# Kernel tuning notes

Hardware: AMD Instinct MI355X
Metric: run time of the kernel (lower is better)

Reference implementation:

```python
import jax, jax.numpy as jnp
import numpy as np

DIM = 768
N_HEADS = 12
HEAD_DIM = DIM // N_HEADS
HIDDEN = 4 * DIM
EPS = 1e-5


def _layernorm(x, gamma, beta):
    mu = jnp.mean(x, axis=-1, keepdims=True)
    var = jnp.mean(jnp.square(x - mu), axis=-1, keepdims=True)
    return (x - mu) * jax.lax.rsqrt(var + EPS) * gamma + beta


def setup_inputs() -> dict:
    key = jax.random.key(0)
    ks = jax.random.split(key, 8)
    B, N = 16, 1024
    s = 0.02
    return {
        "x": jax.random.normal(ks[0], (B, N, DIM), jnp.float32),
        "Wqkv": jax.random.normal(ks[1], (DIM, 3 * DIM), jnp.float32) * s,
        "bqkv": jnp.zeros((3 * DIM,), jnp.float32),
        "Wproj": jax.random.normal(ks[2], (DIM, DIM), jnp.float32) * s,
        "bproj": jnp.zeros((DIM,), jnp.float32),
        "g1": jnp.ones((DIM,), jnp.float32),
        "b1": jnp.zeros((DIM,), jnp.float32),
        "g2": jnp.ones((DIM,), jnp.float32),
        "b2": jnp.zeros((DIM,), jnp.float32),
        "W1": jax.random.normal(ks[3], (DIM, HIDDEN), jnp.float32) * s,
        "bf1": jnp.zeros((HIDDEN,), jnp.float32),
        "W2": jax.random.normal(ks[4], (HIDDEN, DIM), jnp.float32) * s,
        "bf2": jnp.zeros((DIM,), jnp.float32),
    }


def reference(x, Wqkv, bqkv, Wproj, bproj, g1, b1, g2, b2, W1, bf1, W2, bf2):
    B, N, _ = x.shape
    # --- attention branch (pre-LN) ---
    h = _layernorm(x, g1, b1)
    qkv = (h @ Wqkv + bqkv).reshape(B, N, 3, N_HEADS, HEAD_DIM)
    qkv = jnp.transpose(qkv, (2, 0, 3, 1, 4))  # [3, B, H, N, D]
    q, k, v = qkv[0], qkv[1], qkv[2]
    # NOTE: source scales by dim**-0.5, not head_dim**-0.5 (faithful)
    scores = jnp.einsum("bhnd,bhmd->bhnm", q, k) * (DIM ** -0.5)
    attn = jax.nn.softmax(scores, axis=-1)
    out = jnp.einsum("bhnm,bhmd->bhnd", attn, v)
    out = jnp.transpose(out, (0, 2, 1, 3)).reshape(B, N, DIM)
    x = x + (out @ Wproj + bproj)
    # --- MLP branch ---
    h2 = _layernorm(x, g2, b2)
    ff = jax.nn.relu(h2 @ W1 + bf1) @ W2 + bf2
    return x + ff
```

## Files before the change

kernel.cpp:

```cpp
#include <hip/hip_runtime.h>
#include <cstdint>
#include <cstddef>

typedef unsigned short u16;
typedef __bf16 bf16x8 __attribute__((ext_vector_type(8)));
typedef unsigned short u16x8 __attribute__((ext_vector_type(8)));
typedef float f32x4 __attribute__((ext_vector_type(4)));

#define DIMN 768
#define BNROWS 16384
#define NH 12
#define HD 64
#define HID 3072
#define QKVN 2304

__device__ __forceinline__ u16 f2bf(float f) {
  unsigned u = __builtin_bit_cast(unsigned, f);
  u += 0x7fffu + ((u >> 16) & 1u);
  return (u16)(u >> 16);
}

__device__ __forceinline__ bf16x8 ld8(const u16* p) {
  u16x8 v = *reinterpret_cast<const u16x8*>(p);
  return __builtin_bit_cast(bf16x8, v);
}

__device__ __forceinline__ void gload16(const void* g, void* l) {
  __builtin_amdgcn_global_load_lds(
      (const __attribute__((address_space(1))) unsigned int*)g,
      (__attribute__((address_space(3))) unsigned int*)l, 16, 0, 0);
}

#define MFMA(a, b, c) __builtin_amdgcn_mfma_f32_16x16x32_bf16(a, b, c, 0, 0, 0)

__global__ __launch_bounds__(256) void twb_k(const float* __restrict__ W,
                                             u16* __restrict__ Wt, int K, int N) {
  __shared__ float tile[32][33];
  const int n0 = blockIdx.x * 32, k0 = blockIdx.y * 32;
  const int tx = threadIdx.x & 31, ty = threadIdx.x >> 5;
#pragma unroll
  for (int i = 0; i < 4; i++)
    tile[ty + i * 8][tx] = W[(size_t)(k0 + ty + i * 8) * N + n0 + tx];
  __syncthreads();
#pragma unroll
  for (int i = 0; i < 4; i++)
    Wt[(size_t)(n0 + ty + i * 8) * K + k0 + tx] = f2bf(tile[tx][ty + i * 8]);
}

__global__ __launch_bounds__(256) void ln_k(const float* __restrict__ x,
                                            const float* __restrict__ g,
                                            const float* __restrict__ bta,
                                            u16* __restrict__ outp) {
  const int row = blockIdx.x * 4 + (threadIdx.x >> 6);
  const int lane = threadIdx.x & 63;
  const float4* xr = (const float4*)(x + (size_t)row * DIMN);
  float4 v[3];
  float s = 0.f, ss = 0.f;
#pragma unroll
  for (int c = 0; c < 3; c++) {
    v[c] = xr[c * 64 + lane];
    s += v[c].x + v[c].y + v[c].z + v[c].w;
    ss += v[c].x * v[c].x + v[c].y * v[c].y + v[c].z * v[c].z + v[c].w * v[c].w;
  }
#pragma unroll
  for (int off = 1; off < 64; off <<= 1) {
    s += __shfl_xor(s, off);
    ss += __shfl_xor(ss, off);
  }
  const float mu = s * (1.f / DIMN);
  const float var = ss * (1.f / DIMN) - mu * mu;
  const float rs = rsqrtf(var + 1e-5f);
  u16* orow = outp + (size_t)row * DIMN;
#pragma unroll
  for (int c = 0; c < 3; c++) {
    float4 gv = ((const float4*)g)[c * 64 + lane];
    float4 bv = ((const float4*)bta)[c * 64 + lane];
    ushort4 o;
    o.x = f2bf((v[c].x - mu) * rs * gv.x + bv.x);
    o.y = f2bf((v[c].y - mu) * rs * gv.y + bv.y);
    o.z = f2bf((v[c].z - mu) * rs * gv.z + bv.z);
    o.w = f2bf((v[c].w - mu) * rs * gv.w + bv.w);
    ((ushort4*)orow)[c * 64 + lane] = o;
  }
}

template <int OUT_BF16, int RELU, int RESID>
__global__ __launch_bounds__(512, 2) void gemm256_k(const u16* __restrict__ A,
                                                    const u16* __restrict__ Bt,
                                                    const float* __restrict__ bias,
                                                    const float* __restrict__ resid,
                                                    void* __restrict__ Cout, int N, int K) {
  __shared__ u16 lds[65536];
  const int tid = threadIdx.x;
  const int m0 = blockIdx.x * 256;
  const int n0 = blockIdx.y * 256;
  const int lane = tid & 63, w = tid >> 6;
  const int wr = w >> 2, wc = w & 3;
  const int lhi = lane >> 4, llo = lane & 15;
  const int rdoff = (lhi ^ ((llo >> 1) & 3)) * 16;
  const int NT = K >> 5;

  const int srow = tid >> 2;
  const int sc8 = ((tid & 3) ^ ((srow >> 1) & 3)) * 8;
  const u16* aS0 = A + (size_t)(m0 + srow) * K + sc8;
  const u16* aS1 = A + (size_t)(m0 + 128 + srow) * K + sc8;
  const u16* bS0 = Bt + (size_t)(n0 + srow) * K + sc8;
  const u16* bS1 = Bt + (size_t)(n0 + 128 + srow) * K + sc8;

  auto slotBase = [&](int t) -> const char* { return (const char*)lds + ((size_t)(t & 3) << 15); };
  auto stageA = [&](int t) {
    char* sb = (char*)lds + ((size_t)(t & 3) << 15);
    gload16(aS0 + t * 32, sb + tid * 16);
    gload16(aS1 + t * 32, sb + 8192 + tid * 16);
  };
  auto stageB = [&](int t) {
    char* sb = (char*)lds + ((size_t)(t & 3) << 15) + 16384;
    gload16(bS0 + t * 32, sb + tid * 16);
    gload16(bS1 + t * 32, sb + 8192 + tid * 16);
  };

  f32x4 acc[8][4] = {};
  bf16x8 a03[2][4], bfr[2][4], a47[4];

  stageB(0); stageA(0);
  stageB(1); stageA(1);
  stageB(2); stageA(2);
  asm volatile("s_waitcnt vmcnt(8)" ::: "memory");
  __builtin_amdgcn_s_barrier();
  {
    const char* sb = slotBase(0);
#pragma unroll
    for (int ni = 0; ni < 4; ni++)
      bfr[0][ni] = ld8((const u16*)(sb + 16384 + (wc * 64 + ni * 16 + llo) * 64 + rdoff));
#pragma unroll
    for (int mi = 0; mi < 4; mi++)
      a03[0][mi] = ld8((const u16*)(sb + (wr * 128 + mi * 16 + llo) * 64 + rdoff));
  }

#define G256_P1(T, CUR)                                                                  \
  {                                                                                      \
    const char* sbp = slotBase(T);                                                       \
    _Pragma("unroll") for (int mi = 0; mi < 4; mi++)                                     \
        a47[mi] = ld8((const u16*)(sbp + (wr * 128 + (4 + mi) * 16 + llo) * 64 + rdoff));\
    if ((T) + 3 < NT) stageB((T) + 3);                                                   \
    if ((T) + 3 < NT) {                                                                  \
      asm volatile("s_waitcnt vmcnt(6)" ::: "memory");                                   \
    } else if ((T) + 2 < NT) {                                                           \
      asm volatile("s_waitcnt vmcnt(4)" ::: "memory");                                   \
    } else if ((T) + 1 < NT) {                                                           \
      asm volatile("s_waitcnt vmcnt(0)" ::: "memory");                                   \
    }                                                                                    \
    __builtin_amdgcn_s_barrier();                                                        \
    asm volatile("s_waitcnt lgkmcnt(4)" ::: "memory");                                   \
    __builtin_amdgcn_sched_barrier(0);                                                   \
    __builtin_amdgcn_s_setprio(1);                                                       \
    _Pragma("unroll") for (int mi = 0; mi < 4; mi++)                                     \
        _Pragma("unroll") for (int ni = 0; ni < 4; ni++)                                 \
            acc[mi][ni] = MFMA(a03[CUR][mi], bfr[CUR][ni], acc[mi][ni]);                 \
    __builtin_amdgcn_s_setprio(0);                                                       \
    __builtin_amdgcn_sched_barrier(0);                                                   \
  }

#define G256_P2(T, CUR, NXT)                                                             \
  {                                                                                      \
    if ((T) + 1 < NT) {                                                                  \
      const char* sbn = slotBase((T) + 1);                                               \
      _Pragma("unroll") for (int ni = 0; ni < 4; ni++)                                   \
          bfr[NXT][ni] =                                                                 \
              ld8((const u16*)(sbn + 16384 + (wc * 64 + ni * 16 + llo) * 64 + rdoff));   \
      _Pragma("unroll") for (int mi = 0; mi < 4; mi++)                                   \
          a03[NXT][mi] = ld8((const u16*)(sbn + (wr * 128 + mi * 16 + llo) * 64 + rdoff));\
    }                                                                                    \
    if ((T) + 3 < NT) stageA((T) + 3);                                                   \
    __builtin_amdgcn_s_barrier();                                                        \
    if ((T) + 1 < NT) {                                                                  \
      asm volatile("s_waitcnt lgkmcnt(8)" ::: "memory");                                 \
    } else {                                                                             \
      asm volatile("s_waitcnt lgkmcnt(0)" ::: "memory");                                 \
    }                                                                                    \
    __builtin_amdgcn_sched_barrier(0);                                                   \
    __builtin_amdgcn_s_setprio(1);                                                       \
    _Pragma("unroll") for (int mi = 0; mi < 4; mi++)                                     \
        _Pragma("unroll") for (int ni = 0; ni < 4; ni++)                                 \
            acc[4 + mi][ni] = MFMA(a47[mi], bfr[CUR][ni], acc[4 + mi][ni]);              \
    __builtin_amdgcn_s_setprio(0);                                                       \
    __builtin_amdgcn_sched_barrier(0);                                                   \
  }

  for (int t = 0; t < NT; t += 2) {
    G256_P1(t, 0)
    G256_P2(t, 0, 1)
    G256_P1(t + 1, 1)
    G256_P2(t + 1, 1, 0)
  }
#undef G256_P1
#undef G256_P2

#pragma unroll
  for (int mi = 0; mi < 8; mi++)
#pragma unroll
    for (int ni = 0; ni < 4; ni++) {
      const int row = m0 + wr * 128 + mi * 16 + lhi * 4;
      const int col = n0 + wc * 64 + ni * 16 + llo;
      const float bsv = bias[col];
#pragma unroll
      for (int rr = 0; rr < 4; rr++) {
        float v = acc[mi][ni][rr] + bsv;
        if (RELU) v = fmaxf(v, 0.0f);
        const size_t idx = (size_t)(row + rr) * N + col;
        if (RESID) v += resid[idx];
        if (OUT_BF16)
          ((u16*)Cout)[idx] = f2bf(v);
        else
          ((float*)Cout)[idx] = v;
      }
    }
}

template <int OUT_BF16, int RELU, int RESID>
__global__ __launch_bounds__(256, 2) void gemmP_k(const u16* __restrict__ A,
                                                  const u16* __restrict__ Bt,
                                                  const float* __restrict__ bias,
                                                  const float* __restrict__ resid,
                                                  void* __restrict__ Cout, int N, int K) {
  __shared__ u16 lds[3 * 12288];
  const int tid = threadIdx.x;
  const int m0 = blockIdx.x * 256;
  const int n0 = blockIdx.y * 128;
  const int lane = tid & 63, w = tid >> 6;
  const int wr = w >> 1, wc = w & 1;
  const int lhi = lane >> 4, llo = lane & 15;
  const int rdoff = (lhi ^ ((llo >> 1) & 3)) * 16;
  const int NT = K >> 5;

  const int crow = tid >> 2;
  const int kc8 = ((tid & 3) ^ ((crow >> 1) & 3)) * 8;
  const u16* aS = A + (size_t)(m0 + crow) * K + kc8;
  const u16* bS = Bt + (size_t)(n0 + crow) * K + kc8;
  const size_t a64 = (size_t)64 * K;

  auto slotBase = [&](int t) -> const char* { return (const char*)lds + (size_t)(t % 3) * 24576; };
  auto stage1 = [&](int t) {
    char* sb = (char*)lds + (size_t)(t % 3) * 24576;
    gload16(aS + t * 32, sb + tid * 16);
    gload16(aS + a64 + t * 32, sb + 4096 + tid * 16);
    gload16(bS + t * 32, sb + 16384 + tid * 16);
  };
  auto stage2 = [&](int t) {
    char* sb = (char*)lds + (size_t)(t % 3) * 24576;
    gload16(aS + 2 * a64 + t * 32, sb + 8192 + tid * 16);
    gload16(aS + 3 * a64 + t * 32, sb + 12288 + tid * 16);
    gload16(bS + a64 + t * 32, sb + 16384 + 4096 + tid * 16);
  };

  f32x4 acc[8][4] = {};
  bf16x8 a03[2][4], bfr[2][4], a47[4];

  stage1(0); stage2(0);
  stage1(1); stage2(1);
  asm volatile("s_waitcnt vmcnt(6)" ::: "memory");
  __builtin_amdgcn_s_barrier();
  {
    const char* sb = slotBase(0);
#pragma unroll
    for (int ni = 0; ni < 4; ni++)
      bfr[0][ni] = ld8((const u16*)(sb + 16384 + (wc * 64 + ni * 16 + llo) * 64 + rdoff));
#pragma unroll
    for (int mi = 0; mi < 4; mi++)
      a03[0][mi] = ld8((const u16*)(sb + (wr * 128 + mi * 16 + llo) * 64 + rdoff));
  }

#define GP_P1(T, CUR)                                                                    \
  {                                                                                      \
    const char* sbp = slotBase(T);                                                       \
    _Pragma("unroll") for (int mi = 0; mi < 4; mi++)                                     \
        a47[mi] = ld8((const u16*)(sbp + (wr * 128 + (4 + mi) * 16 + llo) * 64 + rdoff));\
    if ((T) + 2 < NT) stage1((T) + 2);                                                   \
    if ((T) + 2 < NT) {                                                                  \
      asm volatile("s_waitcnt vmcnt(3)" ::: "memory");                                   \
    } else if ((T) + 1 < NT) {                                                           \
      asm volatile("s_waitcnt vmcnt(0)" ::: "memory");                                   \
    }                                                                                    \
    __builtin_amdgcn_s_barrier();                                                        \
    asm volatile("s_waitcnt lgkmcnt(4)" ::: "memory");                                   \
    __builtin_amdgcn_sched_barrier(0);                                                   \
    __builtin_amdgcn_s_setprio(1);                                                       \
    _Pragma("unroll") for (int mi = 0; mi < 4; mi++)                                     \
        _Pragma("unroll") for (int ni = 0; ni < 4; ni++)                                 \
            acc[mi][ni] = MFMA(a03[CUR][mi], bfr[CUR][ni], acc[mi][ni]);                 \
    __builtin_amdgcn_s_setprio(0);                                                       \
    __builtin_amdgcn_sched_barrier(0);                                                   \
  }

#define GP_P2(T, CUR, NXT)                                                               \
  {                                                                                      \
    if ((T) + 1 < NT) {                                                                  \
      const char* sbn = slotBase((T) + 1);                                               \
      _Pragma("unroll") for (int ni = 0; ni < 4; ni++)                                   \
          bfr[NXT][ni] =                                                                 \
              ld8((const u16*)(sbn + 16384 + (wc * 64 + ni * 16 + llo) * 64 + rdoff));   \
      _Pragma("unroll") for (int mi = 0; mi < 4; mi++)                                   \
          a03[NXT][mi] = ld8((const u16*)(sbn + (wr * 128 + mi * 16 + llo) * 64 + rdoff));\
    }                                                                                    \
    if ((T) + 2 < NT) stage2((T) + 2);                                                   \
    __builtin_amdgcn_s_barrier();                                                        \
    if ((T) + 1 < NT) {                                                                  \
      asm volatile("s_waitcnt lgkmcnt(8)" ::: "memory");                                 \
    } else {                                                                             \
      asm volatile("s_waitcnt lgkmcnt(0)" ::: "memory");                                 \
    }                                                                                    \
    __builtin_amdgcn_sched_barrier(0);                                                   \
    __builtin_amdgcn_s_setprio(1);                                                       \
    _Pragma("unroll") for (int mi = 0; mi < 4; mi++)                                     \
        _Pragma("unroll") for (int ni = 0; ni < 4; ni++)                                 \
            acc[4 + mi][ni] = MFMA(a47[mi], bfr[CUR][ni], acc[4 + mi][ni]);              \
    __builtin_amdgcn_s_setprio(0);                                                       \
    __builtin_amdgcn_sched_barrier(0);                                                   \
  }

  for (int t = 0; t < NT; t += 2) {
    GP_P1(t, 0)
    GP_P2(t, 0, 1)
    GP_P1(t + 1, 1)
    GP_P2(t + 1, 1, 0)
  }
#undef GP_P1
#undef GP_P2

#pragma unroll
  for (int mi = 0; mi < 8; mi++)
#pragma unroll
    for (int ni = 0; ni < 4; ni++) {
      const int row = m0 + wr * 128 + mi * 16 + lhi * 4;
      const int col = n0 + wc * 64 + ni * 16 + llo;
      const float bsv = bias[col];
#pragma unroll
      for (int rr = 0; rr < 4; rr++) {
        float v = acc[mi][ni][rr] + bsv;
        if (RELU) v = fmaxf(v, 0.0f);
        const size_t idx = (size_t)(row + rr) * N + col;
        if (RESID) v += resid[idx];
        if (OUT_BF16)
          ((u16*)Cout)[idx] = f2bf(v);
        else
          ((float*)Cout)[idx] = v;
      }
    }
}

__device__ __forceinline__ bf16x8 ldscale8(const u16* p, float c) {
  u16x8 v = *reinterpret_cast<const u16x8*>(p);
  bf16x8 r;
#pragma unroll
  for (int j = 0; j < 8; j++) {
    float f = __builtin_bit_cast(float, (unsigned)v[j] << 16) * c;
    r[j] = (__bf16)f;
  }
  return r;
}

__device__ __forceinline__ unsigned pack_bf2(float a, float b) {
  unsigned ua = (unsigned)__builtin_bit_cast(u16, (__bf16)a);
  unsigned ub = (unsigned)__builtin_bit_cast(u16, (__bf16)b);
  return ua | (ub << 16);
}

__global__ __launch_bounds__(256, 3) void attn_k(const u16* __restrict__ qkv,
                                                 u16* __restrict__ outp) {
  __shared__ u16 Ks[2][64 * 64];
  __shared__ u16 Vt[2][64 * 64];
  __shared__ u16 Ps[4][32 * 64];

  const int tid = threadIdx.x;
  const int f = blockIdx.x;
  const int bh = (f & 7) | ((f >> 6) << 3);
  const int qt = (f >> 3) & 7;
  const int b = bh / NH, h = bh - b * NH;
  const int lane = tid & 63, w = tid >> 6;
  const int lhi = lane >> 4, llo = lane & 15;
  const size_t rowb = (size_t)b * 1024;
  const int wq0 = qt * 128 + w * 32;
  const float SC = 0.052059750f;

  bf16x8 qb[2][2];
#pragma unroll
  for (int mi = 0; mi < 2; mi++) {
    const u16* qrow = qkv + (rowb + wq0 + mi * 16 + llo) * QKVN + h * HD;
    qb[mi][0] = ldscale8(qrow + lhi * 8, SC);
    qb[mi][1] = ldscale8(qrow + 32 + lhi * 8, SC);
  }

  bf16x8 ones;
#pragma unroll
  for (int j = 0; j < 8; j++) ones[j] = (__bf16)1.0f;

  const u16* kbase = qkv + rowb * QKVN + DIMN + h * HD;
  const u16* vbase = qkv + rowb * QKVN + 2 * DIMN + h * HD;
  const int sw = (llo & 7) * 8;
  const int rsw = llo & 7;

  const int srow = tid >> 3, su = tid & 7;
  const u16* ksrc = kbase + (size_t)srow * QKVN + (su ^ (srow & 7)) * 8;
  auto stageK = [&](int kt, int slot) {
    const u16* s0 = ksrc + (size_t)kt * 64 * QKVN;
    gload16(s0, (char*)&Ks[slot][0] + tid * 16);
    gload16(s0 + (size_t)32 * QKVN, (char*)&Ks[slot][0] + 4096 + tid * 16);
  };

  const int vp = (lane & 31) * 2;
  const int dc = w * 8 + (lane >> 5) * 32;
  auto loadV = [&](int kt, u16x8& a, u16x8& c) {
    const u16* vr = vbase + (size_t)(kt * 64 + vp) * QKVN + dc;
    a = *reinterpret_cast<const u16x8*>(vr);
    c = *reinterpret_cast<const u16x8*>(vr + QKVN);
  };
  auto writeV = [&](int buf, u16x8 a, u16x8 c) {
#pragma unroll
    for (int j = 0; j < 8; j++) {
      unsigned val = (unsigned)a[j] | ((unsigned)c[j] << 16);
      *reinterpret_cast<unsigned*>(&Vt[buf][(dc + j) * 64 + (vp ^ (j * 8))]) = val;
    }
  };

  u16x8 v0, v1, nv0, nv1;

  stageK(0, 0);
  loadV(0, v0, v1);
  stageK(1, 1);
  asm volatile("s_waitcnt vmcnt(2)" ::: "memory");
  writeV(0, v0, v1);
  asm volatile("s_waitcnt lgkmcnt(0)" ::: "memory");
  __builtin_amdgcn_s_barrier();
  __builtin_amdgcn_sched_barrier(0);

  f32x4 oacc[2][4] = {};
  f32x4 racc[2] = {};

  for (int t = 0; t < 16; t++) {
    if (t < 15) loadV(t + 1, nv0, nv1);

    const u16* kB = &Ks[t & 1][0];
    f32x4 sacc[4][2] = {};
#pragma unroll
    for (int ks = 0; ks < 2; ks++)
#pragma unroll
      for (int ni = 0; ni < 4; ni++) {
        bf16x8 kf = ld8(&kB[(ni * 16 + llo) * 64 + (((ks * 4 + lhi) ^ rsw) * 8)]);
#pragma unroll
        for (int mi = 0; mi < 2; mi++) sacc[ni][mi] = MFMA(kf, qb[mi][ks], sacc[ni][mi]);
      }

    asm volatile("s_waitcnt lgkmcnt(0)" ::: "memory");
    __builtin_amdgcn_s_barrier();
    __builtin_amdgcn_sched_barrier(0);
    if (t + 2 < 16) stageK(t + 2, t & 1);

#pragma unroll
    for (int mi = 0; mi < 2; mi++)
#pragma unroll
      for (int ni = 0; ni < 4; ni++) {
        float p0 = __builtin_amdgcn_exp2f(sacc[ni][mi][0]);
        float p1 = __builtin_amdgcn_exp2f(sacc[ni][mi][1]);
        float p2 = __builtin_amdgcn_exp2f(sacc[ni][mi][2]);
        float p3 = __builtin_amdgcn_exp2f(sacc[ni][mi][3]);
        u16* pp = &Ps[w][(mi * 16 + llo) * 64 + ((ni * 16 + lhi * 4) ^ sw)];
        uint2 pw;
        pw.x = pack_bf2(p0, p1);
        pw.y = pack_bf2(p2, p3);
        *reinterpret_cast<uint2*>(pp) = pw;
      }

#pragma unroll
    for (int ks = 0; ks < 2; ks++) {
      const int koff = ks * 32 + lhi * 8;
      bf16x8 pa0 = ld8(&Ps[w][llo * 64 + (koff ^ sw)]);
      bf16x8 pa1 = ld8(&Ps[w][(16 + llo) * 64 + (koff ^ sw)]);
#pragma unroll
      for (int ni = 0; ni < 4; ni++) {
        bf16x8 vb = ld8(&Vt[t & 1][(ni * 16 + llo) * 64 + (koff ^ sw)]);
        oacc[0][ni] = MFMA(pa0, vb, oacc[0][ni]);
        oacc[1][ni] = MFMA(pa1, vb, oacc[1][ni]);
      }
      racc[0] = MFMA(pa0, ones, racc[0]);
      racc[1] = MFMA(pa1, ones, racc[1]);
    }

    if (t < 15) {
      if (t + 2 < 16) {
        asm volatile("s_waitcnt vmcnt(2)" ::: "memory");
      } else {
        asm volatile("s_waitcnt vmcnt(0)" ::: "memory");
      }
      writeV((t + 1) & 1, nv0, nv1);
      v0 = nv0; v1 = nv1;
      asm volatile("s_waitcnt lgkmcnt(0)" ::: "memory");
      __builtin_amdgcn_s_barrier();
      __builtin_amdgcn_sched_barrier(0);
    }
  }

#pragma unroll
  for (int mi = 0; mi < 2; mi++)
#pragma unroll
    for (int ni = 0; ni < 4; ni++)
#pragma unroll
      for (int r = 0; r < 4; r++) {
        const size_t row = rowb + wq0 + mi * 16 + lhi * 4 + r;
        outp[row * DIMN + h * HD + ni * 16 + llo] = f2bf(oacc[mi][ni][r] / racc[mi][r]);
      }
}

extern "C" void kernel_launch(void* const* d_in, const int* in_sizes, int n_in,
                              void* d_out, int out_size, void* d_ws, size_t ws_size,
                              hipStream_t stream) {
  const float* x = (const float*)d_in[0];
  const float* Wqkv = (const float*)d_in[1];
  const float* bqkv = (const float*)d_in[2];
  const float* Wproj = (const float*)d_in[3];
  const float* bproj = (const float*)d_in[4];
  const float* g1 = (const float*)d_in[5];
  const float* b1 = (const float*)d_in[6];
  const float* g2 = (const float*)d_in[7];
  const float* b2 = (const float*)d_in[8];
  const float* W1 = (const float*)d_in[9];
  const float* bf1 = (const float*)d_in[10];
  const float* W2 = (const float*)d_in[11];
  const float* bf2 = (const float*)d_in[12];
  float* outp = (float*)d_out;

  char* p = (char*)d_ws;
  u16* WqkvT = (u16*)p; p += (size_t)QKVN * DIMN * 2;
  u16* WprojT = (u16*)p; p += (size_t)DIMN * DIMN * 2;
  u16* W1T = (u16*)p; p += (size_t)HID * DIMN * 2;
  u16* W2T = (u16*)p; p += (size_t)DIMN * HID * 2;
  u16* bufX = (u16*)p; p += (size_t)BNROWS * DIMN * 2;
  u16* big = (u16*)p; p += (size_t)BNROWS * HID * 2;

  twb_k<<<dim3(QKVN / 32, DIMN / 32), 256, 0, stream>>>(Wqkv, WqkvT, DIMN, QKVN);
  twb_k<<<dim3(DIMN / 32, DIMN / 32), 256, 0, stream>>>(Wproj, WprojT, DIMN, DIMN);
  twb_k<<<dim3(HID / 32, DIMN / 32), 256, 0, stream>>>(W1, W1T, DIMN, HID);
  twb_k<<<dim3(DIMN / 32, HID / 32), 256, 0, stream>>>(W2, W2T, HID, DIMN);

  ln_k<<<BNROWS / 4, 256, 0, stream>>>(x, g1, b1, bufX);
  gemm256_k<1, 0, 0><<<dim3(64, QKVN / 256), 512, 0, stream>>>(bufX, WqkvT, bqkv, nullptr,
                                                               big, QKVN, DIMN);
  attn_k<<<1536, 256, 0, stream>>>(big, bufX);
  gemmP_k<0, 0, 1><<<dim3(64, DIMN / 128), 256, 0, stream>>>(bufX, WprojT, bproj, x, outp,
                                                             DIMN, DIMN);
  ln_k<<<BNROWS / 4, 256, 0, stream>>>(outp, g2, b2, bufX);
  gemm256_k<1, 1, 0><<<dim3(64, HID / 256), 512, 0, stream>>>(bufX, W1T, bf1, nullptr, big,
                                                              HID, DIMN);
  gemmP_k<0, 0, 1><<<dim3(64, DIMN / 128), 256, 0, stream>>>(big, W2T, bf2, outp, outp,
                                                             DIMN, HID);
}
```

Measured before the change: 426.4 us.

## Restructure 256x256 GEMM main loop to two-slot steps and stage fp32 epilogue via LDS

The first GEMM kernel's split A/B staging with interleaved half-tile MFMA phases is replaced by a simpler loop. Each iteration loads full A and B fragments for two K-slots, waits on LDS, runs all 32 MFMAs per slot, and issues global prefetches two slots at a time with a four-deep ring. Separately, the second GEMM kernel's fp32-output epilogue now stages accumulators through LDS per wave so it can write coalesced float4 stores with vectorized bias and residual reads. The simpler schedule gives up finer-grained overlap of LDS reads with MFMA, which may expose LDS latency, in exchange for fewer barriers and waits.

```diff
diff --git a/kernel.cpp b/kernel.cpp
--- a/kernel.cpp
+++ b/kernel.cpp
@@ -108,93 +108,67 @@
   const u16* bS1 = Bt + (size_t)(n0 + 128 + srow) * K + sc8;
 
   auto slotBase = [&](int t) -> const char* { return (const char*)lds + ((size_t)(t & 3) << 15); };
-  auto stageA = [&](int t) {
+  auto stageAB = [&](int t) {
     char* sb = (char*)lds + ((size_t)(t & 3) << 15);
     gload16(aS0 + t * 32, sb + tid * 16);
     gload16(aS1 + t * 32, sb + 8192 + tid * 16);
+    gload16(bS0 + t * 32, sb + 16384 + tid * 16);
+    gload16(bS1 + t * 32, sb + 16384 + 8192 + tid * 16);
   };
-  auto stageB = [&](int t) {
-    char* sb = (char*)lds + ((size_t)(t & 3) << 15) + 16384;
-    gload16(bS0 + t * 32, sb + tid * 16);
-    gload16(bS1 + t * 32, sb + 8192 + tid * 16);
-  };
 
   f32x4 acc[8][4] = {};
-  bf16x8 a03[2][4], bfr[2][4], a47[4];
-
-  stageB(0); stageA(0);
-  stageB(1); stageA(1);
-  stageB(2); stageA(2);
+  bf16x8 af[8], bfr[4];
+
+  stageAB(0);
+  stageAB(1);
+  stageAB(2);
+  stageAB(3);
   asm volatile("s_waitcnt vmcnt(8)" ::: "memory");
   __builtin_amdgcn_s_barrier();
-  {
-    const char* sb = slotBase(0);
+
+  for (int T = 0; T < NT; T += 2) {
+    const char* s0 = slotBase(T);
+    const char* s1 = slotBase(T + 1);
 #pragma unroll
     for (int ni = 0; ni < 4; ni++)
-      bfr[0][ni] = ld8((const u16*)(sb + 16384 + (wc * 64 + ni * 16 + llo) * 64 + rdoff));
-#pragma unroll
-    for (int mi = 0; mi < 4; mi++)
-      a03[0][mi] = ld8((const u16*)(sb + (wr * 128 + mi * 16 + llo) * 64 + rdoff));
-  }
-
-#define G256_P1(T, CUR)                                                                  \
-  {                                                                                      \
-    const char* sbp = slotBase(T);                                                       \
-    _Pragma("unroll") for (int mi = 0; mi < 4; mi++)                                     \
-        a47[mi] = ld8((const u16*)(sbp + (wr * 128 + (4 + mi) * 16 + llo) * 64 + rdoff));\
-    if ((T) + 3 < NT) stageB((T) + 3);                                                   \
-    if ((T) + 3 < NT) {                                                                  \
-      asm volatile("s_waitcnt vmcnt(6)" ::: "memory");                                   \
-    } else if ((T) + 2 < NT) {                                                           \
-      asm volatile("s_waitcnt vmcnt(4)" ::: "memory");                                   \
-    } else if ((T) + 1 < NT) {                                                           \
-      asm volatile("s_waitcnt vmcnt(0)" ::: "memory");                                   \
-    }                                                                                    \
-    __builtin_amdgcn_s_barrier();                                                        \
-    asm volatile("s_waitcnt lgkmcnt(4)" ::: "memory");                                   \
-    __builtin_amdgcn_sched_barrier(0);                                                   \
-    __builtin_amdgcn_s_setprio(1);                                                       \
-    _Pragma("unroll") for (int mi = 0; mi < 4; mi++)                                     \
-        _Pragma("unroll") for (int ni = 0; ni < 4; ni++)                                 \
-            acc[mi][ni] = MFMA(a03[CUR][mi], bfr[CUR][ni], acc[mi][ni]);                 \
-    __builtin_amdgcn_s_setprio(0);                                                       \
-    __builtin_amdgcn_sched_barrier(0);                                                   \
-  }
-
-#define G256_P2(T, CUR, NXT)                                                             \
-  {                                                                                      \
-    if ((T) + 1 < NT) {                                                                  \
-      const char* sbn = slotBase((T) + 1);                                               \
-      _Pragma("unroll") for (int ni = 0; ni < 4; ni++)                                   \
-          bfr[NXT][ni] =                                                                 \
-              ld8((const u16*)(sbn + 16384 + (wc * 64 + ni * 16 + llo) * 64 + rdoff));   \
-      _Pragma("unroll") for (int mi = 0; mi < 4; mi++)                                   \
-          a03[NXT][mi] = ld8((const u16*)(sbn + (wr * 128 + mi * 16 + llo) * 64 + rdoff));\
-    }                                                                                    \
-    if ((T) + 3 < NT) stageA((T) + 3);                                                   \
-    __builtin_amdgcn_s_barrier();                                                        \
-    if ((T) + 1 < NT) {                                                                  \
-      asm volatile("s_waitcnt lgkmcnt(8)" ::: "memory");                                 \
-    } else {                                                                             \
-      asm volatile("s_waitcnt lgkmcnt(0)" ::: "memory");                                 \
-    }                                                                                    \
-    __builtin_amdgcn_sched_barrier(0);                                                   \
-    __builtin_amdgcn_s_setprio(1);                                                       \
-    _Pragma("unroll") for (int mi = 0; mi < 4; mi++)                                     \
-        _Pragma("unroll") for (int ni = 0; ni < 4; ni++)                                 \
-            acc[4 + mi][ni] = MFMA(a47[mi], bfr[CUR][ni], acc[4 + mi][ni]);              \
-    __builtin_amdgcn_s_setprio(0);                                                       \
-    __builtin_amdgcn_sched_barrier(0);                                                   \
-  }
-
-  for (int t = 0; t < NT; t += 2) {
-    G256_P1(t, 0)
-    G256_P2(t, 0, 1)
-    G256_P1(t + 1, 1)
-    G256_P2(t + 1, 1, 0)
-  }
-#undef G256_P1
-#undef G256_P2
+      bfr[ni] = ld8((const u16*)(s0 + 16384 + (wc * 64 + ni * 16 + llo) * 64 + rdoff));
+#pragma unroll
+    for (int mi = 0; mi < 8; mi++)
+      af[mi] = ld8((const u16*)(s0 + (wr * 128 + mi * 16 + llo) * 64 + rdoff));
+    asm volatile("s_waitcnt lgkmcnt(0)" ::: "memory");
+    __builtin_amdgcn_sched_barrier(0);
+    __builtin_amdgcn_s_setprio(1);
+#pragma unroll
+    for (int mi = 0; mi < 8; mi++)
+#pragma unroll
+      for (int ni = 0; ni < 4; ni++) acc[mi][ni] = MFMA(af[mi], bfr[ni], acc[mi][ni]);
+    __builtin_amdgcn_s_setprio(0);
+    __builtin_amdgcn_sched_barrier(0);
+#pragma unroll
+    for (int ni = 0; ni < 4; ni++)
+      bfr[ni] = ld8((const u16*)(s1 + 16384 + (wc * 64 + ni * 16 + llo) * 64 + rdoff));
+#pragma unroll
+    for (int mi = 0; mi < 8; mi++)
+      af[mi] = ld8((const u16*)(s1 + (wr * 128 + mi * 16 + llo) * 64 + rdoff));
+    asm volatile("s_waitcnt lgkmcnt(0)" ::: "memory");
+    __builtin_amdgcn_sched_barrier(0);
+    __builtin_amdgcn_s_barrier();
+    if (T + 4 < NT) stageAB(T + 4);
+    if (T + 5 < NT) stageAB(T + 5);
+    __builtin_amdgcn_s_setprio(1);
+#pragma unroll
+    for (int mi = 0; mi < 8; mi++)
+#pragma unroll
+      for (int ni = 0; ni < 4; ni++) acc[mi][ni] = MFMA(af[mi], bfr[ni], acc[mi][ni]);
+    __builtin_amdgcn_s_setprio(0);
+    __builtin_amdgcn_sched_barrier(0);
+    if (T + 4 < NT) {
+      asm volatile("s_waitcnt vmcnt(8)" ::: "memory");
+    } else if (T + 2 < NT) {
+      asm volatile("s_waitcnt vmcnt(0)" ::: "memory");
+    }
+    __builtin_amdgcn_s_barrier();
+  }
 
 #pragma unroll
   for (int mi = 0; mi < 8; mi++)
@@ -327,25 +301,61 @@
 #undef GP_P1
 #undef GP_P2
 
-#pragma unroll
-  for (int mi = 0; mi < 8; mi++)
-#pragma unroll
-    for (int ni = 0; ni < 4; ni++) {
-      const int row = m0 + wr * 128 + mi * 16 + lhi * 4;
-      const int col = n0 + wc * 64 + ni * 16 + llo;
-      const float bsv = bias[col];
-#pragma unroll
-      for (int rr = 0; rr < 4; rr++) {
-        float v = acc[mi][ni][rr] + bsv;
-        if (RELU) v = fmaxf(v, 0.0f);
-        const size_t idx = (size_t)(row + rr) * N + col;
-        if (RESID) v += resid[idx];
-        if (OUT_BF16)
+  if constexpr (!OUT_BF16) {
+    float* ep = (float*)lds + (size_t)w * 2176;
+    const int r0 = lane >> 2;
+    const int fc = (lane & 3) * 16;
+#pragma unroll
+    for (int c = 0; c < 4; c++) {
+#pragma unroll
+      for (int dmi = 0; dmi < 2; dmi++)
+#pragma unroll
+        for (int ni = 0; ni < 4; ni++)
+#pragma unroll
+          for (int rr = 0; rr < 4; rr++)
+            ep[(dmi * 16 + lhi * 4 + rr) * 68 + ni * 16 + llo] = acc[2 * c + dmi][ni][rr];
+#pragma unroll
+      for (int half = 0; half < 2; half++) {
+        const int r = r0 + half * 16;
+        const int grow = m0 + wr * 128 + c * 32 + r;
+        const int gcol = n0 + wc * 64 + fc;
+        float* gp = (float*)Cout + (size_t)grow * N + gcol;
+        const float* rp = resid + (size_t)grow * N + gcol;
+#pragma unroll
+        for (int j = 0; j < 4; j++) {
+          float4 v = *(float4*)&ep[r * 68 + fc + 4 * j];
+          float4 bv = *(const float4*)&bias[gcol + 4 * j];
+          v.x += bv.x; v.y += bv.y; v.z += bv.z; v.w += bv.w;
+          if (RELU) {
+            v.x = fmaxf(v.x, 0.f); v.y = fmaxf(v.y, 0.f);
+            v.z = fmaxf(v.z, 0.f); v.w = fmaxf(v.w, 0.f);
+          }
+          if (RESID) {
+            float4 rv = ((const float4*)rp)[j];
+            v.x += rv.x; v.y += rv.y; v.z += rv.z; v.w += rv.w;
+          }
+          ((float4*)gp)[j] = v;
+        }
+      }
+    }
+  } else {
+#pragma unroll
+    for (int mi = 0; mi < 8; mi++)
+#pragma unroll
+      for (int ni = 0; ni < 4; ni++) {
+        const int row = m0 + wr * 128 + mi * 16 + lhi * 4;
+        const int col = n0 + wc * 64 + ni * 16 + llo;
+        const float bsv = bias[col];
+#pragma unroll
+        for (int rr = 0; rr < 4; rr++) {
+          float v = acc[mi][ni][rr] + bsv;
+          if (RELU) v = fmaxf(v, 0.0f);
+          const size_t idx = (size_t)(row + rr) * N + col;
+          if (RESID) v += resid[idx];
           ((u16*)Cout)[idx] = f2bf(v);
-        else
-          ((float*)Cout)[idx] = v;
-      }
-    }
+        }
+      }
+  }
 }
 
 __device__ __forceinline__ bf16x8 ldscale8(const u16* p, float c) {
```

After: 453.5 us. +6.4%, slower.
